# Performance work log

Hardware: AMD Instinct MI355X
Metric: run time of the kernel (lower is better)

Reference implementation:

```python
import jax, jax.numpy as jnp
import numpy as np

B, S, HID, H = 4, 2048, 1024, 8
D = HID // H  # per-head dim = 128


def setup_inputs() -> dict:
    key = jax.random.key(0)
    ks = jax.random.split(key, 8)
    q = jax.random.normal(ks[0], (B, S, HID), dtype=jnp.float32)
    k = jax.random.normal(ks[1], (B, S, HID), dtype=jnp.float32)
    v = jax.random.normal(ks[2], (B, S, HID), dtype=jnp.float32)
    mask = jax.random.randint(ks[3], (B, S), 0, 2, dtype=jnp.int32)  # 1 = masked key
    # Linear(hidden, hidden, bias=False) weights, stored [in, out] so y = x @ W
    xavier = lambda kk: jax.random.uniform(kk, (HID, HID), jnp.float32,
                                           -np.sqrt(6.0 / (2 * HID)), np.sqrt(6.0 / (2 * HID)))
    return {"q": q, "k": k, "v": v, "mask": mask,
            "Wq": xavier(ks[4]), "Wk": xavier(ks[5]), "Wv": xavier(ks[6]), "Wo": xavier(ks[7])}


def reference(q, k, v, mask, Wq, Wk, Wv, Wo):
    scale = D ** -0.5
    # project and split heads: [B,S,HID] -> [B,H,S,D]
    qq = (q @ Wq).reshape(B, S, H, D).transpose(0, 2, 1, 3) * scale
    kk = (k @ Wk).reshape(B, S, H, D).transpose(0, 2, 1, 3)
    vv = (v @ Wv).reshape(B, S, H, D).transpose(0, 2, 1, 3)
    # scores [B,H,Sq,Sk]; mask broadcasts over heads and query rows (key padding)
    scores = jnp.einsum('bhqd,bhkd->bhqk', qq, kk)
    scores = jnp.where(mask.astype(bool)[:, None, None, :], jnp.float32(-1e9), scores)
    attn = jax.nn.softmax(scores, axis=-1)  # dropout_rate=0 (eval) -> identity
    ctx = jnp.einsum('bhqk,bhkd->bhqd', attn, vv)
    out = ctx.transpose(0, 2, 1, 3).reshape(B, S, HID) @ Wo
    return out, attn
```

## Files before the change

kernel.cpp:

```cpp
#include <hip/hip_runtime.h>
#include <hip/hip_bf16.h>

#define HIDN 1024
#define NH   8
#define DH   128
#define BB   4
#define SS   2048

typedef __bf16 bf16;
typedef bf16 bf16x4 __attribute__((ext_vector_type(4)));
typedef bf16 bf16x8 __attribute__((ext_vector_type(8)));
typedef float f32x4 __attribute__((ext_vector_type(4)));

#if __has_builtin(__builtin_amdgcn_exp2f)
#define EXP2(x) __builtin_amdgcn_exp2f(x)
#else
#define EXP2(x) exp2f(x)
#endif

static __device__ inline f32x4 mfma16(bf16x8 a, bf16x8 b, f32x4 c) {
    return __builtin_amdgcn_mfma_f32_16x16x32_bf16(a, b, c, 0, 0, 0);
}

static __device__ inline void gload_lds16(const void* g, void* l) {
    __builtin_amdgcn_global_load_lds(
        (const __attribute__((address_space(1))) unsigned int*)g,
        (__attribute__((address_space(3))) unsigned int*)l, 16, 0, 0);
}

__global__ void cvt_kernel(const float* __restrict__ q, const float* __restrict__ k,
                           const float* __restrict__ v,
                           bf16* __restrict__ qo, bf16* __restrict__ ko, bf16* __restrict__ vo) {
    const float* src = blockIdx.y == 0 ? q : blockIdx.y == 1 ? k : v;
    bf16* dst = blockIdx.y == 0 ? qo : blockIdx.y == 1 ? ko : vo;
    const size_t n = (size_t)BB * SS * HIDN;
    for (size_t i = ((size_t)blockIdx.x * blockDim.x + threadIdx.x) * 8; i < n;
         i += (size_t)gridDim.x * blockDim.x * 8) {
        float4 a = *(const float4*)&src[i];
        float4 b = *(const float4*)&src[i + 4];
        bf16x8 o = {(bf16)a.x, (bf16)a.y, (bf16)a.z, (bf16)a.w,
                    (bf16)b.x, (bf16)b.y, (bf16)b.z, (bf16)b.w};
        *(bf16x8*)&dst[i] = o;
    }
}

__global__ void wconv_kernel(const float* __restrict__ W0, const float* __restrict__ W1,
                             const float* __restrict__ W2, const float* __restrict__ W3,
                             bf16* __restrict__ O) {
    const float* W = blockIdx.z == 0 ? W0 : blockIdx.z == 1 ? W1 : blockIdx.z == 2 ? W2 : W3;
    bf16* WT = O + (size_t)blockIdx.z * HIDN * HIDN;
    int nb = blockIdx.x * 64;
    int kb = blockIdx.y * 64;
    int t = threadIdx.x;
    __shared__ bf16 tile[64][72];
    {
        int r = t >> 2, cp = (t & 3) * 16;
        #pragma unroll
        for (int j = 0; j < 16; j += 4) {
            float4 val = *(const float4*)&W[(size_t)(kb + r) * HIDN + nb + cp + j];
            tile[r][cp + j + 0] = (bf16)val.x;
            tile[r][cp + j + 1] = (bf16)val.y;
            tile[r][cp + j + 2] = (bf16)val.z;
            tile[r][cp + j + 3] = (bf16)val.w;
        }
    }
    __syncthreads();
    {
        int n = t >> 2, kp = (t & 3) * 16;
        bf16 o[16];
        #pragma unroll
        for (int j = 0; j < 16; ++j) o[j] = tile[kp + j][n];
        #pragma unroll
        for (int j = 0; j < 2; ++j)
            *(bf16x8*)&WT[(size_t)(nb + n) * HIDN + kb + kp + j * 8] = *(bf16x8*)&o[j * 8];
    }
}

template <int OUTMODE>
static __device__ inline void gemm_core(const bf16* __restrict__ A, const bf16* __restrict__ Bt,
                                        void* __restrict__ Cp, float alpha, char* smem) {
    int orig = blockIdx.x + blockIdx.y * gridDim.x;
    int virt = (orig & 7) * 64 + (orig >> 3);
    int bm = (virt & 63) * 128;
    int bn = (virt >> 6) * 128;
    int t = threadIdx.x;
    int wave = t >> 6, lane = t & 63;
    int wr = wave >> 1, wc = wave & 1;
    int lr = lane & 15, lg = lane >> 4;
    int so = wave * 1024 + lane * 16;
    f32x4 acc[4][4] = {};

    auto stage = [&](int k0, char* buf) {
        #pragma unroll
        for (int i = 0; i < 4; ++i) {
            int o = i * 4096 + so;
            int r = o >> 7, cb = o & 127;
            int cbs = cb ^ ((r & 7) << 4);
            gload_lds16(&A[(size_t)(bm + r) * HIDN + k0 + (cbs >> 1)], buf + i * 4096 + wave * 1024);
            gload_lds16(&Bt[(size_t)(bn + r) * HIDN + k0 + (cbs >> 1)], buf + 16384 + i * 4096 + wave * 1024);
        }
    };
    stage(0, smem);
    for (int kt = 0; kt < 16; ++kt) {
        const char* cur = smem + (kt & 1) * 32768;
        char* nxt = smem + ((kt & 1) ^ 1) * 32768;
        asm volatile("s_waitcnt vmcnt(0)" ::: "memory");
        __builtin_amdgcn_s_barrier();
        if (kt < 15) stage((kt + 1) * 64, nxt);
        asm volatile("" ::: "memory");
        #pragma unroll
        for (int kd = 0; kd < 2; ++kd) {
            bf16x8 af[4], bfr[4];
            #pragma unroll
            for (int mi = 0; mi < 4; ++mi) {
                int row = wr * 64 + mi * 16 + lr;
                int cb = (kd * 64 + lg * 16) ^ ((row & 7) << 4);
                af[mi] = *(const bf16x8*)(cur + row * 128 + cb);
            }
            #pragma unroll
            for (int ni = 0; ni < 4; ++ni) {
                int row = wc * 64 + ni * 16 + lr;
                int cb = (kd * 64 + lg * 16) ^ ((row & 7) << 4);
                bfr[ni] = *(const bf16x8*)(cur + 16384 + row * 128 + cb);
            }
            #pragma unroll
            for (int mi = 0; mi < 4; ++mi)
                #pragma unroll
                for (int ni = 0; ni < 4; ++ni)
                    acc[mi][ni] = mfma16(af[mi], bfr[ni], acc[mi][ni]);
        }
    }
    if constexpr (OUTMODE == 2) {
        __syncthreads();
        bf16* tile_t = (bf16*)smem;
        #pragma unroll
        for (int mi = 0; mi < 4; ++mi)
            #pragma unroll
            for (int ni = 0; ni < 4; ++ni) {
                bf16x4 o = {(bf16)acc[mi][ni][0], (bf16)acc[mi][ni][1],
                            (bf16)acc[mi][ni][2], (bf16)acc[mi][ni][3]};
                *(bf16x4*)&tile_t[(wc * 64 + ni * 16 + lr) * 136 + wr * 64 + mi * 16 + lg * 4] = o;
            }
        __syncthreads();
        int d = t >> 1, sh = (t & 1) * 64;
        int b = bm >> 11, h = bn >> 7;
        bf16* vvT = (bf16*)Cp;
        size_t base = ((size_t)(b * NH + h) * DH + d) * SS + (bm & 2047) + sh;
        #pragma unroll
        for (int j = 0; j < 8; ++j)
            *(bf16x8*)&vvT[base + j * 8] = *(const bf16x8*)&tile_t[d * 136 + sh + j * 8];
    } else {
        #pragma unroll
        for (int mi = 0; mi < 4; ++mi)
            #pragma unroll
            for (int ni = 0; ni < 4; ++ni)
                #pragma unroll
                for (int r = 0; r < 4; ++r) {
                    int row = bm + wr * 64 + mi * 16 + lg * 4 + r;
                    int col = bn + wc * 64 + ni * 16 + lr;
                    if constexpr (OUTMODE == 0)
                        ((bf16*)Cp)[(size_t)row * HIDN + col] = (bf16)(acc[mi][ni][r] * alpha);
                    else
                        ((float*)Cp)[(size_t)row * HIDN + col] = acc[mi][ni][r] * alpha;
                }
    }
}

__global__ __launch_bounds__(256, 2)
void proj_gemm_kernel(const bf16* __restrict__ qb, const bf16* __restrict__ kb,
                      const bf16* __restrict__ vb, const bf16* __restrict__ Wall,
                      bf16* __restrict__ qq, bf16* __restrict__ kk, bf16* __restrict__ vvT,
                      float qalpha) {
    __shared__ __align__(16) char smem[65536];
    int z = blockIdx.z;
    const bf16* Bt = Wall + (size_t)z * HIDN * HIDN;
    if (z == 2)      gemm_core<2>(vb, Bt, vvT, 1.0f, smem);
    else if (z == 1) gemm_core<0>(kb, Bt, kk, 1.0f, smem);
    else             gemm_core<0>(qb, Bt, qq, qalpha, smem);
}

__global__ __launch_bounds__(256, 2)
void out_gemm_kernel(const bf16* __restrict__ A, const bf16* __restrict__ Bt,
                     float* __restrict__ C) {
    __shared__ __align__(16) char smem[65536];
    gemm_core<1>(A, Bt, C, 1.0f, smem);
}

static __device__ inline void stage_k(const bf16* kbase, int kt, char* Ksm, int wave, int lane) {
    #pragma unroll
    for (int i = 0; i < 8; ++i) {
        int o = i * 4096 + wave * 1024 + lane * 16;
        int r = o >> 8, cb = o & 255;
        int cbs = cb ^ ((r & 15) << 4);
        gload_lds16(&kbase[(size_t)(kt * 128 + r) * HIDN + (cbs >> 1)],
                    Ksm + i * 4096 + wave * 1024);
    }
}

static __device__ inline bf16x8 read_k(const char* Ksm, int row, int cstart_bytes) {
    int cb = cstart_bytes ^ ((row & 15) << 4);
    return *(const bf16x8*)(Ksm + row * 256 + cb);
}

__global__ __launch_bounds__(256, 2)
void attn_fused_kernel(const bf16* __restrict__ qq, const bf16* __restrict__ kk,
                       const bf16* __restrict__ vvT, const int* __restrict__ mask,
                       float* __restrict__ attn, bf16* __restrict__ ctx) {
    __shared__ __align__(16) char smem[67584];
    char* K0 = smem;
    char* K1 = smem + 32768;
    bf16(*P)[136] = (bf16(*)[136])(smem + 32768);
    float* slf = (float*)(smem + 32768);

    int orig = blockIdx.x + blockIdx.y * gridDim.x;
    int virt = (orig & 7) * 64 + (orig >> 3);
    int qt = virt & 15, bh = virt >> 4;
    int b = bh >> 3, h = bh & 7;
    int t = threadIdx.x;
    int wave = t >> 6, lane = t & 63;
    int wr = wave >> 1, wc = wave & 1;
    int lr = lane & 15, lg = lane >> 4;

    const bf16* qbase = qq + (size_t)b * SS * HIDN + h * DH;
    const bf16* kbase = kk + (size_t)b * SS * HIDN + h * DH;
    const int* mbase = mask + b * SS;

    bf16x8 qf[4][4];
    #pragma unroll
    for (int mi = 0; mi < 4; ++mi)
        #pragma unroll
        for (int kd = 0; kd < 4; ++kd)
            qf[mi][kd] = *(const bf16x8*)&qbase[(size_t)(qt * 128 + wr * 64 + mi * 16 + lr) * HIDN + kd * 32 + lg * 8];

    unsigned long long mkbits = 0;
    #pragma unroll
    for (int kt = 0; kt < 16; ++kt)
        #pragma unroll
        for (int ni = 0; ni < 4; ++ni)
            mkbits |= (unsigned long long)(mbase[kt * 128 + wc * 64 + ni * 16 + lr] != 0)
                      << (kt * 4 + ni);

    float l_[16] = {};
    stage_k(kbase, 0, K0, wave, lane);
    for (int kt = 0; kt < 16; ++kt) {
        const char* cur = (kt & 1) ? K1 : K0;
        char* nxt = (kt & 1) ? K0 : K1;
        __syncthreads();
        if (kt < 15) stage_k(kbase, kt + 1, nxt, wave, lane);
        f32x4 acc[4][4] = {};
        #pragma unroll
        for (int kd = 0; kd < 4; ++kd) {
            bf16x8 kf[4];
            #pragma unroll
            for (int ni = 0; ni < 4; ++ni)
                kf[ni] = read_k(cur, wc * 64 + ni * 16 + lr, kd * 64 + lg * 16);
            #pragma unroll
            for (int mi = 0; mi < 4; ++mi)
                #pragma unroll
                for (int ni = 0; ni < 4; ++ni)
                    acc[mi][ni] = mfma16(qf[mi][kd], kf[ni], acc[mi][ni]);
        }
        #pragma unroll
        for (int mi = 0; mi < 4; ++mi)
            #pragma unroll
            for (int r = 0; r < 4; ++r) {
                int s = mi * 4 + r;
                float v0 = ((mkbits >> (kt * 4 + 0)) & 1) ? -1e9f : acc[mi][0][r];
                float v1 = ((mkbits >> (kt * 4 + 1)) & 1) ? -1e9f : acc[mi][1][r];
                float v2 = ((mkbits >> (kt * 4 + 2)) & 1) ? -1e9f : acc[mi][2][r];
                float v3 = ((mkbits >> (kt * 4 + 3)) & 1) ? -1e9f : acc[mi][3][r];
                l_[s] += (EXP2(v0 - 12.f) + EXP2(v1 - 12.f)) + (EXP2(v2 - 12.f) + EXP2(v3 - 12.f));
            }
    }

    stage_k(kbase, 0, K0, wave, lane);

    #pragma unroll
    for (int o = 1; o < 16; o <<= 1)
        #pragma unroll
        for (int s = 0; s < 16; ++s) l_[s] += __shfl_xor(l_[s], o);
    __syncthreads();
    if (lr == 0) {
        #pragma unroll
        for (int mi = 0; mi < 4; ++mi)
            #pragma unroll
            for (int r = 0; r < 4; ++r)
                slf[wc * 128 + wr * 64 + mi * 16 + lg * 4 + r] = l_[mi * 4 + r];
    }
    __syncthreads();
    float rl[16];
    #pragma unroll
    for (int mi = 0; mi < 4; ++mi)
        #pragma unroll
        for (int r = 0; r < 4; ++r) {
            int row = wr * 64 + mi * 16 + lg * 4 + r;
            rl[mi * 4 + r] = 1.0f / (slf[row] + slf[128 + row]);
        }
    __syncthreads();

    f32x4 cacc[4][4] = {};
    for (int kt = 0; kt < 16; ++kt) {
        f32x4 acc[4][4] = {};
        #pragma unroll
        for (int kd = 0; kd < 4; ++kd) {
            bf16x8 kf[4];
            #pragma unroll
            for (int ni = 0; ni < 4; ++ni)
                kf[ni] = read_k(K0, wc * 64 + ni * 16 + lr, kd * 64 + lg * 16);
            #pragma unroll
            for (int mi = 0; mi < 4; ++mi)
                #pragma unroll
                for (int ni = 0; ni < 4; ++ni)
                    acc[mi][ni] = mfma16(qf[mi][kd], kf[ni], acc[mi][ni]);
        }
        #pragma unroll
        for (int mi = 0; mi < 4; ++mi)
            #pragma unroll
            for (int ni = 0; ni < 4; ++ni)
                #pragma unroll
                for (int r = 0; r < 4; ++r) {
                    float s = ((mkbits >> (kt * 4 + ni)) & 1) ? -1e9f : acc[mi][ni][r];
                    float p = EXP2(s - 12.f) * rl[mi * 4 + r];
                    int rowl = wr * 64 + mi * 16 + lg * 4 + r;
                    int coll = wc * 64 + ni * 16 + lr;
                    P[rowl][coll] = (bf16)p;
                    __builtin_nontemporal_store(
                        p, &attn[((size_t)bh * SS + qt * 128 + rowl) * SS + kt * 128 + coll]);
                }
        __syncthreads();
        if (kt < 15) stage_k(kbase, kt + 1, K0, wave, lane);
        #pragma unroll
        for (int ks = 0; ks < 4; ++ks) {
            bf16x8 pf[4], vf[4];
            #pragma unroll
            for (int mi = 0; mi < 4; ++mi)
                pf[mi] = *(const bf16x8*)&P[wr * 64 + mi * 16 + lr][ks * 32 + lg * 8];
            #pragma unroll
            for (int ni = 0; ni < 4; ++ni)
                vf[ni] = *(const bf16x8*)&vvT[((size_t)bh * DH + wc * 64 + ni * 16 + lr) * SS + kt * 128 + ks * 32 + lg * 8];
            #pragma unroll
            for (int mi = 0; mi < 4; ++mi)
                #pragma unroll
                for (int ni = 0; ni < 4; ++ni)
                    cacc[mi][ni] = mfma16(pf[mi], vf[ni], cacc[mi][ni]);
        }
        __syncthreads();
    }

    #pragma unroll
    for (int mi = 0; mi < 4; ++mi)
        #pragma unroll
        for (int ni = 0; ni < 4; ++ni)
            #pragma unroll
            for (int r = 0; r < 4; ++r)
                P[wr * 64 + mi * 16 + lg * 4 + r][wc * 64 + ni * 16 + lr] = (bf16)cacc[mi][ni][r];
    __syncthreads();
    {
        int row = t >> 1, half = (t & 1) * 64;
        bf16* dst = ctx + ((size_t)b * SS + qt * 128 + row) * HIDN + h * DH + half;
        #pragma unroll
        for (int j = 0; j < 8; ++j)
            *(bf16x8*)&dst[j * 8] = *(const bf16x8*)&P[row][half + j * 8];
    }
}

extern "C" void kernel_launch(void* const* d_in, const int* in_sizes, int n_in,
                              void* d_out, int out_size, void* d_ws, size_t ws_size,
                              hipStream_t stream) {
    const float* q = (const float*)d_in[0];
    const float* k = (const float*)d_in[1];
    const float* v = (const float*)d_in[2];
    const int* mask = (const int*)d_in[3];
    const float* Wq = (const float*)d_in[4];
    const float* Wk = (const float*)d_in[5];
    const float* Wv = (const float*)d_in[6];
    const float* Wo = (const float*)d_in[7];
    (void)in_sizes; (void)n_in; (void)out_size; (void)ws_size;

    float* outp = (float*)d_out;
    float* attn = outp + (size_t)BB * SS * HIDN;

    char* ws = (char*)d_ws;
    size_t off = 0;
    auto alloc = [&](size_t bytes) { char* p = ws + off; off += (bytes + 255) & ~(size_t)255; return p; };
    const size_t wbytes = (size_t)HIDN * HIDN * sizeof(bf16);
    const size_t tbytes = (size_t)BB * SS * HIDN * sizeof(bf16);
    bf16* WmatT = (bf16*)alloc(4 * wbytes);
    bf16* qbf = (bf16*)alloc(tbytes);
    bf16* kbf = (bf16*)alloc(tbytes);
    bf16* vbf = (bf16*)alloc(tbytes);
    bf16* qqb = (bf16*)alloc(tbytes);
    bf16* kkb = (bf16*)alloc(tbytes);
    bf16* vvTb = (bf16*)alloc(tbytes);
    bf16* ctxb = qbf;
    bf16* WoT = WmatT + 3 * (size_t)HIDN * HIDN;

    dim3 blk(256);
    cvt_kernel<<<dim3(1024, 3), blk, 0, stream>>>(q, k, v, qbf, kbf, vbf);
    wconv_kernel<<<dim3(16, 16, 4), blk, 0, stream>>>(Wq, Wk, Wv, Wo, WmatT);

    const float qalpha = 0.12751744f;
    proj_gemm_kernel<<<dim3(64, 8, 3), blk, 0, stream>>>(qbf, kbf, vbf, WmatT,
                                                         qqb, kkb, vvTb, qalpha);

    attn_fused_kernel<<<dim3(16, 32), blk, 0, stream>>>(qqb, kkb, vvTb, mask, attn, ctxb);

    out_gemm_kernel<<<dim3(64, 8), blk, 0, stream>>>(ctxb, WoT, outp);
}
```

Before: 361.1 us.

## Split attention into single-pass PV kernel and separate probability writer kernel

Replaces the two-pass fused attention kernel with two kernels. The first computes unnormalized exp scores, the row sums and P·V in a single pass over K with 64-row tiles and a double-buffered LDS pipeline using explicit waitcnt and setprio, then normalizes ctx at the end and saves the reciprocal row sums. The second recomputes QK^T over split key halves and writes the normalized attention probabilities. This decouples the large attention-matrix write from the PV MMA work and raises occupancy through smaller tiles, at the cost of recomputing QK^T and an extra launch.

Measured after the change: 456.3 us. 26.4% more time.

```diff
diff --git a/kernel.cpp b/kernel.cpp
--- a/kernel.cpp
+++ b/kernel.cpp
@@ -186,14 +186,14 @@
     gemm_core<1>(A, Bt, C, 1.0f, smem);
 }
 
-static __device__ inline void stage_k(const bf16* kbase, int kt, char* Ksm, int wave, int lane) {
-    #pragma unroll
-    for (int i = 0; i < 8; ++i) {
+static __device__ inline void stage64(const bf16* kb, int row0, char* buf, int wave, int lane) {
+    #pragma unroll
+    for (int i = 0; i < 4; ++i) {
         int o = i * 4096 + wave * 1024 + lane * 16;
         int r = o >> 8, cb = o & 255;
         int cbs = cb ^ ((r & 15) << 4);
-        gload_lds16(&kbase[(size_t)(kt * 128 + r) * HIDN + (cbs >> 1)],
-                    Ksm + i * 4096 + wave * 1024);
+        gload_lds16(&kb[(size_t)(row0 + r) * HIDN + (cbs >> 1)],
+                    buf + i * 4096 + wave * 1024);
     }
 }
 
@@ -202,19 +202,18 @@
     return *(const bf16x8*)(Ksm + row * 256 + cb);
 }
 
-__global__ __launch_bounds__(256, 2)
-void attn_fused_kernel(const bf16* __restrict__ qq, const bf16* __restrict__ kk,
-                       const bf16* __restrict__ vvT, const int* __restrict__ mask,
-                       float* __restrict__ attn, bf16* __restrict__ ctx) {
-    __shared__ __align__(16) char smem[67584];
-    char* K0 = smem;
-    char* K1 = smem + 32768;
-    bf16(*P)[136] = (bf16(*)[136])(smem + 32768);
+__global__ __launch_bounds__(256, 3)
+void attn_pv_kernel(const bf16* __restrict__ qq, const bf16* __restrict__ kk,
+                    const bf16* __restrict__ vvT, const int* __restrict__ mask,
+                    float* __restrict__ rlg, bf16* __restrict__ ctx) {
+    __shared__ __align__(16) char smem[42240];
+    char* Kbuf = smem;
+    bf16(*P)[72] = (bf16(*)[72])(smem + 32768);
     float* slf = (float*)(smem + 32768);
 
-    int orig = blockIdx.x + blockIdx.y * gridDim.x;
-    int virt = (orig & 7) * 64 + (orig >> 3);
-    int qt = virt & 15, bh = virt >> 4;
+    int orig = blockIdx.x;
+    int virt = (orig & 7) * 128 + (orig >> 3);
+    int qt = virt & 31, bh = virt >> 5;
     int b = bh >> 3, h = bh & 7;
     int t = threadIdx.x;
     int wave = t >> 6, lane = t & 63;
@@ -225,142 +224,206 @@
     const bf16* kbase = kk + (size_t)b * SS * HIDN + h * DH;
     const int* mbase = mask + b * SS;
 
-    bf16x8 qf[4][4];
-    #pragma unroll
-    for (int mi = 0; mi < 4; ++mi)
+    bf16x8 qf[2][4];
+    #pragma unroll
+    for (int mi = 0; mi < 2; ++mi)
         #pragma unroll
         for (int kd = 0; kd < 4; ++kd)
-            qf[mi][kd] = *(const bf16x8*)&qbase[(size_t)(qt * 128 + wr * 64 + mi * 16 + lr) * HIDN + kd * 32 + lg * 8];
+            qf[mi][kd] = *(const bf16x8*)&qbase[(size_t)(qt * 64 + wr * 32 + mi * 16 + lr) * HIDN + kd * 32 + lg * 8];
 
     unsigned long long mkbits = 0;
     #pragma unroll
-    for (int kt = 0; kt < 16; ++kt)
-        #pragma unroll
-        for (int ni = 0; ni < 4; ++ni)
-            mkbits |= (unsigned long long)(mbase[kt * 128 + wc * 64 + ni * 16 + lr] != 0)
-                      << (kt * 4 + ni);
-
-    float l_[16] = {};
-    stage_k(kbase, 0, K0, wave, lane);
-    for (int kt = 0; kt < 16; ++kt) {
-        const char* cur = (kt & 1) ? K1 : K0;
-        char* nxt = (kt & 1) ? K0 : K1;
-        __syncthreads();
-        if (kt < 15) stage_k(kbase, kt + 1, nxt, wave, lane);
-        f32x4 acc[4][4] = {};
+    for (int kt = 0; kt < 32; ++kt)
+        #pragma unroll
+        for (int ni = 0; ni < 2; ++ni)
+            mkbits |= (unsigned long long)(mbase[kt * 64 + wc * 32 + ni * 16 + lr] != 0)
+                      << (kt * 2 + ni);
+
+    float l_[8] = {};
+    f32x4 cacc[2][4] = {};
+    stage64(kbase, 0, Kbuf, wave, lane);
+    for (int kt = 0; kt < 32; ++kt) {
+        const char* cur = Kbuf + (kt & 1) * 16384;
+        char* nxt = Kbuf + ((kt & 1) ^ 1) * 16384;
+        if (kt == 0) asm volatile("s_waitcnt vmcnt(0)" ::: "memory");
+        else         asm volatile("s_waitcnt vmcnt(8)" ::: "memory");
+        __builtin_amdgcn_s_barrier();
+        if (kt < 31) stage64(kbase, (kt + 1) * 64, nxt, wave, lane);
+        asm volatile("" ::: "memory");
+        f32x4 acc[2][2] = {};
+        __builtin_amdgcn_s_setprio(1);
         #pragma unroll
         for (int kd = 0; kd < 4; ++kd) {
-            bf16x8 kf[4];
+            bf16x8 kf[2];
+            #pragma unroll
+            for (int ni = 0; ni < 2; ++ni)
+                kf[ni] = read_k(cur, wc * 32 + ni * 16 + lr, kd * 64 + lg * 16);
+            #pragma unroll
+            for (int mi = 0; mi < 2; ++mi)
+                #pragma unroll
+                for (int ni = 0; ni < 2; ++ni)
+                    acc[mi][ni] = mfma16(qf[mi][kd], kf[ni], acc[mi][ni]);
+        }
+        __builtin_amdgcn_s_setprio(0);
+        #pragma unroll
+        for (int mi = 0; mi < 2; ++mi)
+            #pragma unroll
+            for (int r = 0; r < 4; ++r) {
+                float v0 = ((mkbits >> (kt * 2 + 0)) & 1) ? -1e9f : acc[mi][0][r];
+                float v1 = ((mkbits >> (kt * 2 + 1)) & 1) ? -1e9f : acc[mi][1][r];
+                float p0 = EXP2(v0 - 12.f);
+                float p1 = EXP2(v1 - 12.f);
+                l_[mi * 4 + r] += p0 + p1;
+                int rowl = wr * 32 + mi * 16 + lg * 4 + r;
+                P[rowl][wc * 32 + lr] = (bf16)p0;
+                P[rowl][wc * 32 + 16 + lr] = (bf16)p1;
+            }
+        asm volatile("s_waitcnt lgkmcnt(0)" ::: "memory");
+        __builtin_amdgcn_s_barrier();
+        __builtin_amdgcn_s_setprio(1);
+        #pragma unroll
+        for (int ks = 0; ks < 2; ++ks) {
+            bf16x8 pf[2], vf[4];
+            #pragma unroll
+            for (int mi = 0; mi < 2; ++mi)
+                pf[mi] = *(const bf16x8*)&P[wr * 32 + mi * 16 + lr][ks * 32 + lg * 8];
             #pragma unroll
             for (int ni = 0; ni < 4; ++ni)
-                kf[ni] = read_k(cur, wc * 64 + ni * 16 + lr, kd * 64 + lg * 16);
-            #pragma unroll
-            for (int mi = 0; mi < 4; ++mi)
-                #pragma unroll
-                for (int ni = 0; ni < 4; ++ni)
-                    acc[mi][ni] = mfma16(qf[mi][kd], kf[ni], acc[mi][ni]);
-        }
-        #pragma unroll
-        for (int mi = 0; mi < 4; ++mi)
-            #pragma unroll
-            for (int r = 0; r < 4; ++r) {
-                int s = mi * 4 + r;
-                float v0 = ((mkbits >> (kt * 4 + 0)) & 1) ? -1e9f : acc[mi][0][r];
-                float v1 = ((mkbits >> (kt * 4 + 1)) & 1) ? -1e9f : acc[mi][1][r];
-                float v2 = ((mkbits >> (kt * 4 + 2)) & 1) ? -1e9f : acc[mi][2][r];
-                float v3 = ((mkbits >> (kt * 4 + 3)) & 1) ? -1e9f : acc[mi][3][r];
-                l_[s] += (EXP2(v0 - 12.f) + EXP2(v1 - 12.f)) + (EXP2(v2 - 12.f) + EXP2(v3 - 12.f));
-            }
-    }
-
-    stage_k(kbase, 0, K0, wave, lane);
-
-    #pragma unroll
-    for (int o = 1; o < 16; o <<= 1)
-        #pragma unroll
-        for (int s = 0; s < 16; ++s) l_[s] += __shfl_xor(l_[s], o);
-    __syncthreads();
-    if (lr == 0) {
-        #pragma unroll
-        for (int mi = 0; mi < 4; ++mi)
-            #pragma unroll
-            for (int r = 0; r < 4; ++r)
-                slf[wc * 128 + wr * 64 + mi * 16 + lg * 4 + r] = l_[mi * 4 + r];
-    }
-    __syncthreads();
-    float rl[16];
-    #pragma unroll
-    for (int mi = 0; mi < 4; ++mi)
-        #pragma unroll
-        for (int r = 0; r < 4; ++r) {
-            int row = wr * 64 + mi * 16 + lg * 4 + r;
-            rl[mi * 4 + r] = 1.0f / (slf[row] + slf[128 + row]);
-        }
-    __syncthreads();
-
-    f32x4 cacc[4][4] = {};
-    for (int kt = 0; kt < 16; ++kt) {
-        f32x4 acc[4][4] = {};
-        #pragma unroll
-        for (int kd = 0; kd < 4; ++kd) {
-            bf16x8 kf[4];
-            #pragma unroll
-            for (int ni = 0; ni < 4; ++ni)
-                kf[ni] = read_k(K0, wc * 64 + ni * 16 + lr, kd * 64 + lg * 16);
-            #pragma unroll
-            for (int mi = 0; mi < 4; ++mi)
-                #pragma unroll
-                for (int ni = 0; ni < 4; ++ni)
-                    acc[mi][ni] = mfma16(qf[mi][kd], kf[ni], acc[mi][ni]);
-        }
-        #pragma unroll
-        for (int mi = 0; mi < 4; ++mi)
-            #pragma unroll
-            for (int ni = 0; ni < 4; ++ni)
-                #pragma unroll
-                for (int r = 0; r < 4; ++r) {
-                    float s = ((mkbits >> (kt * 4 + ni)) & 1) ? -1e9f : acc[mi][ni][r];
-                    float p = EXP2(s - 12.f) * rl[mi * 4 + r];
-                    int rowl = wr * 64 + mi * 16 + lg * 4 + r;
-                    int coll = wc * 64 + ni * 16 + lr;
-                    P[rowl][coll] = (bf16)p;
-                    __builtin_nontemporal_store(
-                        p, &attn[((size_t)bh * SS + qt * 128 + rowl) * SS + kt * 128 + coll]);
-                }
-        __syncthreads();
-        if (kt < 15) stage_k(kbase, kt + 1, K0, wave, lane);
-        #pragma unroll
-        for (int ks = 0; ks < 4; ++ks) {
-            bf16x8 pf[4], vf[4];
-            #pragma unroll
-            for (int mi = 0; mi < 4; ++mi)
-                pf[mi] = *(const bf16x8*)&P[wr * 64 + mi * 16 + lr][ks * 32 + lg * 8];
-            #pragma unroll
-            for (int ni = 0; ni < 4; ++ni)
-                vf[ni] = *(const bf16x8*)&vvT[((size_t)bh * DH + wc * 64 + ni * 16 + lr) * SS + kt * 128 + ks * 32 + lg * 8];
-            #pragma unroll
-            for (int mi = 0; mi < 4; ++mi)
+                vf[ni] = *(const bf16x8*)&vvT[((size_t)bh * DH + wc * 64 + ni * 16 + lr) * SS + kt * 64 + ks * 32 + lg * 8];
+            #pragma unroll
+            for (int mi = 0; mi < 2; ++mi)
                 #pragma unroll
                 for (int ni = 0; ni < 4; ++ni)
                     cacc[mi][ni] = mfma16(pf[mi], vf[ni], cacc[mi][ni]);
         }
-        __syncthreads();
-    }
-
-    #pragma unroll
-    for (int mi = 0; mi < 4; ++mi)
+        __builtin_amdgcn_s_setprio(0);
+    }
+
+    #pragma unroll
+    for (int o = 1; o < 16; o <<= 1)
+        #pragma unroll
+        for (int s = 0; s < 8; ++s) l_[s] += __shfl_xor(l_[s], o);
+    __syncthreads();
+    if (lr == 0) {
+        #pragma unroll
+        for (int mi = 0; mi < 2; ++mi)
+            #pragma unroll
+            for (int r = 0; r < 4; ++r)
+                slf[wc * 64 + wr * 32 + mi * 16 + lg * 4 + r] = l_[mi * 4 + r];
+    }
+    __syncthreads();
+    float rl[8];
+    #pragma unroll
+    for (int mi = 0; mi < 2; ++mi)
+        #pragma unroll
+        for (int r = 0; r < 4; ++r) {
+            int row = wr * 32 + mi * 16 + lg * 4 + r;
+            rl[mi * 4 + r] = 1.0f / (slf[row] + slf[64 + row]);
+        }
+    if (lr == 0) {
+        #pragma unroll
+        for (int mi = 0; mi < 2; ++mi)
+            #pragma unroll
+            for (int r = 0; r < 4; ++r)
+                rlg[(size_t)bh * SS + qt * 64 + wr * 32 + mi * 16 + lg * 4 + r] = rl[mi * 4 + r];
+    }
+
+    bf16(*Ct)[136] = (bf16(*)[136])Kbuf;
+    #pragma unroll
+    for (int mi = 0; mi < 2; ++mi)
         #pragma unroll
         for (int ni = 0; ni < 4; ++ni)
             #pragma unroll
             for (int r = 0; r < 4; ++r)
-                P[wr * 64 + mi * 16 + lg * 4 + r][wc * 64 + ni * 16 + lr] = (bf16)cacc[mi][ni][r];
+                Ct[wr * 32 + mi * 16 + lg * 4 + r][wc * 64 + ni * 16 + lr] =
+                    (bf16)(cacc[mi][ni][r] * rl[mi * 4 + r]);
     __syncthreads();
     {
-        int row = t >> 1, half = (t & 1) * 64;
-        bf16* dst = ctx + ((size_t)b * SS + qt * 128 + row) * HIDN + h * DH + half;
-        #pragma unroll
-        for (int j = 0; j < 8; ++j)
-            *(bf16x8*)&dst[j * 8] = *(const bf16x8*)&P[row][half + j * 8];
+        int row = t >> 2, qtr = (t & 3) * 32;
+        bf16* dst = ctx + ((size_t)b * SS + qt * 64 + row) * HIDN + h * DH + qtr;
+        #pragma unroll
+        for (int j = 0; j < 4; ++j)
+            *(bf16x8*)&dst[j * 8] = *(const bf16x8*)&Ct[row][qtr + j * 8];
+    }
+}
+
+__global__ __launch_bounds__(256, 4)
+void attn_probs_kernel(const bf16* __restrict__ qq, const bf16* __restrict__ kk,
+                       const int* __restrict__ mask, const float* __restrict__ rlg,
+                       float* __restrict__ attn) {
+    __shared__ __align__(16) char smem[32768];
+    int orig = blockIdx.x;
+    int virt = (orig & 7) * 256 + (orig >> 3);
+    int ck = virt & 1, qt = (virt >> 1) & 31, bh = virt >> 6;
+    int b = bh >> 3, h = bh & 7;
+    int t = threadIdx.x;
+    int wave = t >> 6, lane = t & 63;
+    int wr = wave >> 1, wc = wave & 1;
+    int lr = lane & 15, lg = lane >> 4;
+
+    const bf16* qbase = qq + (size_t)b * SS * HIDN + h * DH;
+    const bf16* kbase = kk + (size_t)b * SS * HIDN + h * DH + (size_t)ck * 1024 * HIDN;
+    const int* mbase = mask + b * SS + ck * 1024;
+
+    bf16x8 qf[2][4];
+    #pragma unroll
+    for (int mi = 0; mi < 2; ++mi)
+        #pragma unroll
+        for (int kd = 0; kd < 4; ++kd)
+            qf[mi][kd] = *(const bf16x8*)&qbase[(size_t)(qt * 64 + wr * 32 + mi * 16 + lr) * HIDN + kd * 32 + lg * 8];
+
+    unsigned mkb = 0;
+    #pragma unroll
+    for (int kt = 0; kt < 16; ++kt)
+        #pragma unroll
+        for (int ni = 0; ni < 2; ++ni)
+            mkb |= (unsigned)(mbase[kt * 64 + wc * 32 + ni * 16 + lr] != 0) << (kt * 2 + ni);
+
+    float rl[8];
+    #pragma unroll
+    for (int mi = 0; mi < 2; ++mi)
+        #pragma unroll
+        for (int r = 0; r < 4; ++r)
+            rl[mi * 4 + r] = rlg[(size_t)bh * SS + qt * 64 + wr * 32 + mi * 16 + lg * 4 + r];
+
+    float* abase = attn + ((size_t)bh * SS + qt * 64) * SS + ck * 1024;
+
+    stage64(kbase, 0, smem, wave, lane);
+    for (int kt = 0; kt < 16; ++kt) {
+        const char* cur = smem + (kt & 1) * 16384;
+        char* nxt = smem + ((kt & 1) ^ 1) * 16384;
+        if (kt == 0) asm volatile("s_waitcnt vmcnt(0)" ::: "memory");
+        else         asm volatile("s_waitcnt vmcnt(16)" ::: "memory");
+        __builtin_amdgcn_s_barrier();
+        if (kt < 15) stage64(kbase, (kt + 1) * 64, nxt, wave, lane);
+        asm volatile("" ::: "memory");
+        f32x4 acc[2][2] = {};
+        __builtin_amdgcn_s_setprio(1);
+        #pragma unroll
+        for (int kd = 0; kd < 4; ++kd) {
+            bf16x8 kf[2];
+            #pragma unroll
+            for (int ni = 0; ni < 2; ++ni)
+                kf[ni] = read_k(cur, wc * 32 + ni * 16 + lr, kd * 64 + lg * 16);
+            #pragma unroll
+            for (int mi = 0; mi < 2; ++mi)
+                #pragma unroll
+                for (int ni = 0; ni < 2; ++ni)
+                    acc[mi][ni] = mfma16(qf[mi][kd], kf[ni], acc[mi][ni]);
+        }
+        __builtin_amdgcn_s_setprio(0);
+        #pragma unroll
+        for (int mi = 0; mi < 2; ++mi)
+            #pragma unroll
+            for (int r = 0; r < 4; ++r) {
+                float v0 = ((mkb >> (kt * 2 + 0)) & 1) ? -1e9f : acc[mi][0][r];
+                float v1 = ((mkb >> (kt * 2 + 1)) & 1) ? -1e9f : acc[mi][1][r];
+                float p0 = EXP2(v0 - 12.f) * rl[mi * 4 + r];
+                float p1 = EXP2(v1 - 12.f) * rl[mi * 4 + r];
+                int rowl = wr * 32 + mi * 16 + lg * 4 + r;
+                __builtin_nontemporal_store(p0, &abase[(size_t)rowl * SS + kt * 64 + wc * 32 + lr]);
+                __builtin_nontemporal_store(p1, &abase[(size_t)rowl * SS + kt * 64 + wc * 32 + 16 + lr]);
+            }
     }
 }
 
@@ -392,6 +455,7 @@
     bf16* qqb = (bf16*)alloc(tbytes);
     bf16* kkb = (bf16*)alloc(tbytes);
     bf16* vvTb = (bf16*)alloc(tbytes);
+    float* rlb = (float*)alloc((size_t)BB * NH * SS * sizeof(float));
     bf16* ctxb = qbf;
     bf16* WoT = WmatT + 3 * (size_t)HIDN * HIDN;
 
@@ -403,7 +467,8 @@
     proj_gemm_kernel<<<dim3(64, 8, 3), blk, 0, stream>>>(qbf, kbf, vbf, WmatT,
                                                          qqb, kkb, vvTb, qalpha);
 
-    attn_fused_kernel<<<dim3(16, 32), blk, 0, stream>>>(qqb, kkb, vvTb, mask, attn, ctxb);
+    attn_pv_kernel<<<dim3(1024), blk, 0, stream>>>(qqb, kkb, vvTb, mask, rlb, ctxb);
+    attn_probs_kernel<<<dim3(2048), blk, 0, stream>>>(qqb, kkb, mask, rlb, attn);
 
     out_gemm_kernel<<<dim3(64, 8), blk, 0, stream>>>(ctxb, WoT, outp);
 }
```

## Coalesce attn stores through LDS, prefetch V fragments, add MFMA priority hints

Applied to the files above, without the earlier changes.

The attention probabilities are no longer written straight from MFMA accumulator layout. They are read back from the bf16 P tile in LDS and written as row-contiguous float4 nontemporal stores, so the large attn write goes out in wide coalesced transactions. The V fragments for each key tile are loaded into registers at the top of the iteration, hiding their global latency behind the QK MFMAs. Full __syncthreads are replaced by hand-placed waitcnt/s_barrier, and s_setprio brackets the MFMA sections. In exchange, attn now holds bf16-rounded probabilities, and the hand-written vmcnt counting is fragile.

New measurement: 435.4 us. 20.6% more time.

```diff
diff --git a/kernel.cpp b/kernel.cpp
--- a/kernel.cpp
+++ b/kernel.cpp
@@ -11,6 +11,7 @@
 typedef bf16 bf16x4 __attribute__((ext_vector_type(4)));
 typedef bf16 bf16x8 __attribute__((ext_vector_type(8)));
 typedef float f32x4 __attribute__((ext_vector_type(4)));
+typedef unsigned short u16x4 __attribute__((ext_vector_type(4)));
 
 #if __has_builtin(__builtin_amdgcn_exp2f)
 #define EXP2(x) __builtin_amdgcn_exp2f(x)
@@ -248,6 +249,7 @@
         __syncthreads();
         if (kt < 15) stage_k(kbase, kt + 1, nxt, wave, lane);
         f32x4 acc[4][4] = {};
+        __builtin_amdgcn_s_setprio(1);
         #pragma unroll
         for (int kd = 0; kd < 4; ++kd) {
             bf16x8 kf[4];
@@ -260,6 +262,7 @@
                 for (int ni = 0; ni < 4; ++ni)
                     acc[mi][ni] = mfma16(qf[mi][kd], kf[ni], acc[mi][ni]);
         }
+        __builtin_amdgcn_s_setprio(0);
         #pragma unroll
         for (int mi = 0; mi < 4; ++mi)
             #pragma unroll
@@ -300,7 +303,17 @@
 
     f32x4 cacc[4][4] = {};
     for (int kt = 0; kt < 16; ++kt) {
+        bf16x8 vf[4][4];
+        #pragma unroll
+        for (int ks = 0; ks < 4; ++ks)
+            #pragma unroll
+            for (int ni = 0; ni < 4; ++ni)
+                vf[ks][ni] = *(const bf16x8*)&vvT[((size_t)bh * DH + wc * 64 + ni * 16 + lr) * SS + kt * 128 + ks * 32 + lg * 8];
+        asm volatile("" ::: "memory");
+        asm volatile("s_waitcnt vmcnt(32)" ::: "memory");
+        __builtin_amdgcn_s_barrier();
         f32x4 acc[4][4] = {};
+        __builtin_amdgcn_s_setprio(1);
         #pragma unroll
         for (int kd = 0; kd < 4; ++kd) {
             bf16x8 kf[4];
@@ -313,6 +326,7 @@
                 for (int ni = 0; ni < 4; ++ni)
                     acc[mi][ni] = mfma16(qf[mi][kd], kf[ni], acc[mi][ni]);
         }
+        __builtin_amdgcn_s_setprio(0);
         #pragma unroll
         for (int mi = 0; mi < 4; ++mi)
             #pragma unroll
@@ -321,32 +335,44 @@
                 for (int r = 0; r < 4; ++r) {
                     float s = ((mkbits >> (kt * 4 + ni)) & 1) ? -1e9f : acc[mi][ni][r];
                     float p = EXP2(s - 12.f) * rl[mi * 4 + r];
-                    int rowl = wr * 64 + mi * 16 + lg * 4 + r;
-                    int coll = wc * 64 + ni * 16 + lr;
-                    P[rowl][coll] = (bf16)p;
-                    __builtin_nontemporal_store(
-                        p, &attn[((size_t)bh * SS + qt * 128 + rowl) * SS + kt * 128 + coll]);
+                    P[wr * 64 + mi * 16 + lg * 4 + r][wc * 64 + ni * 16 + lr] = (bf16)p;
                 }
-        __syncthreads();
+        asm volatile("s_waitcnt lgkmcnt(0)" ::: "memory");
+        __builtin_amdgcn_sched_barrier(0);
+        __builtin_amdgcn_s_barrier();
         if (kt < 15) stage_k(kbase, kt + 1, K0, wave, lane);
+        asm volatile("" ::: "memory");
+        {
+            int rw = t >> 5, c4 = (t & 31) * 4;
+            #pragma unroll
+            for (int j = 0; j < 16; ++j) {
+                int row = j * 8 + rw;
+                u16x4 u = *(const u16x4*)&P[row][c4];
+                f32x4 f = {__uint_as_float((unsigned)u.x << 16),
+                           __uint_as_float((unsigned)u.y << 16),
+                           __uint_as_float((unsigned)u.z << 16),
+                           __uint_as_float((unsigned)u.w << 16)};
+                __builtin_nontemporal_store(
+                    f, (f32x4*)(attn + ((size_t)bh * SS + qt * 128 + row) * SS + kt * 128 + c4));
+            }
+        }
+        __builtin_amdgcn_s_setprio(1);
         #pragma unroll
         for (int ks = 0; ks < 4; ++ks) {
-            bf16x8 pf[4], vf[4];
+            bf16x8 pf[4];
             #pragma unroll
             for (int mi = 0; mi < 4; ++mi)
                 pf[mi] = *(const bf16x8*)&P[wr * 64 + mi * 16 + lr][ks * 32 + lg * 8];
             #pragma unroll
-            for (int ni = 0; ni < 4; ++ni)
-                vf[ni] = *(const bf16x8*)&vvT[((size_t)bh * DH + wc * 64 + ni * 16 + lr) * SS + kt * 128 + ks * 32 + lg * 8];
-            #pragma unroll
             for (int mi = 0; mi < 4; ++mi)
                 #pragma unroll
                 for (int ni = 0; ni < 4; ++ni)
-                    cacc[mi][ni] = mfma16(pf[mi], vf[ni], cacc[mi][ni]);
-        }
-        __syncthreads();
-    }
-
+                    cacc[mi][ni] = mfma16(pf[mi], vf[ks][ni], cacc[mi][ni]);
+        }
+        __builtin_amdgcn_s_setprio(0);
+    }
+
+    __syncthreads();
     #pragma unroll
     for (int mi = 0; mi < 4; ++mi)
         #pragma unroll
```

## Read K fragments directly from global memory and drop LDS K staging

Applied to the files above, without the earlier changes.

Removes the double-buffered LDS staging of K tiles and has each wave load its K MFMA fragments straight from global memory (relying on L2/L1 reuse). This shrinks shared memory from about 66KB to 34KB, which could allow higher occupancy. It also brackets MFMA blocks with s_setprio and swaps __syncthreads for raw s_barrier plus an explicit lgkmcnt wait. The trade-off is more, less-coalesced global traffic for K, and a weaker barrier that relies on manual waitcnt to order the P writes in LDS.

New measurement: 422.2 us. +16.9%, slower.

```diff
diff --git a/kernel.cpp b/kernel.cpp
--- a/kernel.cpp
+++ b/kernel.cpp
@@ -186,31 +186,13 @@
     gemm_core<1>(A, Bt, C, 1.0f, smem);
 }
 
-static __device__ inline void stage_k(const bf16* kbase, int kt, char* Ksm, int wave, int lane) {
-    #pragma unroll
-    for (int i = 0; i < 8; ++i) {
-        int o = i * 4096 + wave * 1024 + lane * 16;
-        int r = o >> 8, cb = o & 255;
-        int cbs = cb ^ ((r & 15) << 4);
-        gload_lds16(&kbase[(size_t)(kt * 128 + r) * HIDN + (cbs >> 1)],
-                    Ksm + i * 4096 + wave * 1024);
-    }
-}
-
-static __device__ inline bf16x8 read_k(const char* Ksm, int row, int cstart_bytes) {
-    int cb = cstart_bytes ^ ((row & 15) << 4);
-    return *(const bf16x8*)(Ksm + row * 256 + cb);
-}
-
 __global__ __launch_bounds__(256, 2)
 void attn_fused_kernel(const bf16* __restrict__ qq, const bf16* __restrict__ kk,
                        const bf16* __restrict__ vvT, const int* __restrict__ mask,
                        float* __restrict__ attn, bf16* __restrict__ ctx) {
-    __shared__ __align__(16) char smem[67584];
-    char* K0 = smem;
-    char* K1 = smem + 32768;
-    bf16(*P)[136] = (bf16(*)[136])(smem + 32768);
-    float* slf = (float*)(smem + 32768);
+    __shared__ __align__(16) char smem[34816];
+    bf16(*P)[136] = (bf16(*)[136])smem;
+    float* slf = (float*)smem;
 
     int orig = blockIdx.x + blockIdx.y * gridDim.x;
     int virt = (orig & 7) * 64 + (orig >> 3);
@@ -241,24 +223,21 @@
                       << (kt * 4 + ni);
 
     float l_[16] = {};
-    stage_k(kbase, 0, K0, wave, lane);
     for (int kt = 0; kt < 16; ++kt) {
-        const char* cur = (kt & 1) ? K1 : K0;
-        char* nxt = (kt & 1) ? K0 : K1;
-        __syncthreads();
-        if (kt < 15) stage_k(kbase, kt + 1, nxt, wave, lane);
         f32x4 acc[4][4] = {};
         #pragma unroll
         for (int kd = 0; kd < 4; ++kd) {
             bf16x8 kf[4];
             #pragma unroll
             for (int ni = 0; ni < 4; ++ni)
-                kf[ni] = read_k(cur, wc * 64 + ni * 16 + lr, kd * 64 + lg * 16);
+                kf[ni] = *(const bf16x8*)&kbase[(size_t)(kt * 128 + wc * 64 + ni * 16 + lr) * HIDN + kd * 32 + lg * 8];
+            __builtin_amdgcn_s_setprio(1);
             #pragma unroll
             for (int mi = 0; mi < 4; ++mi)
                 #pragma unroll
                 for (int ni = 0; ni < 4; ++ni)
                     acc[mi][ni] = mfma16(qf[mi][kd], kf[ni], acc[mi][ni]);
+            __builtin_amdgcn_s_setprio(0);
         }
         #pragma unroll
         for (int mi = 0; mi < 4; ++mi)
@@ -273,13 +252,10 @@
             }
     }
 
-    stage_k(kbase, 0, K0, wave, lane);
-
     #pragma unroll
     for (int o = 1; o < 16; o <<= 1)
         #pragma unroll
         for (int s = 0; s < 16; ++s) l_[s] += __shfl_xor(l_[s], o);
-    __syncthreads();
     if (lr == 0) {
         #pragma unroll
         for (int mi = 0; mi < 4; ++mi)
@@ -306,12 +282,14 @@
             bf16x8 kf[4];
             #pragma unroll
             for (int ni = 0; ni < 4; ++ni)
-                kf[ni] = read_k(K0, wc * 64 + ni * 16 + lr, kd * 64 + lg * 16);
+                kf[ni] = *(const bf16x8*)&kbase[(size_t)(kt * 128 + wc * 64 + ni * 16 + lr) * HIDN + kd * 32 + lg * 8];
+            __builtin_amdgcn_s_setprio(1);
             #pragma unroll
             for (int mi = 0; mi < 4; ++mi)
                 #pragma unroll
                 for (int ni = 0; ni < 4; ++ni)
                     acc[mi][ni] = mfma16(qf[mi][kd], kf[ni], acc[mi][ni]);
+            __builtin_amdgcn_s_setprio(0);
         }
         #pragma unroll
         for (int mi = 0; mi < 4; ++mi)
@@ -327,8 +305,10 @@
                     __builtin_nontemporal_store(
                         p, &attn[((size_t)bh * SS + qt * 128 + rowl) * SS + kt * 128 + coll]);
                 }
-        __syncthreads();
-        if (kt < 15) stage_k(kbase, kt + 1, K0, wave, lane);
+        asm volatile("s_waitcnt lgkmcnt(0)" ::: "memory");
+        __builtin_amdgcn_sched_barrier(0);
+        __builtin_amdgcn_s_barrier();
+        __builtin_amdgcn_s_setprio(1);
         #pragma unroll
         for (int ks = 0; ks < 4; ++ks) {
             bf16x8 pf[4], vf[4];
@@ -342,9 +322,10 @@
             for (int mi = 0; mi < 4; ++mi)
                 #pragma unroll
                 for (int ni = 0; ni < 4; ++ni)
-                    cacc[mi][ni] = mfma16(pf[mi], vf[ni], cacc[mi][ni]);
-        }
-        __syncthreads();
+                    cacc[mi][ni] = mfma16(pf[mi], vf[ks == 0 ? ni : ni], cacc[mi][ni]);
+        }
+        __builtin_amdgcn_s_setprio(0);
+        __builtin_amdgcn_s_barrier();
     }
 
     #pragma unroll
```
